# Optimization experiments

Hardware: AMD Instinct MI355X
Metric: run time of the kernel (lower is better)

Reference implementation:

```python
import jax, jax.numpy as jnp
import numpy as np
import math

IMAGE_SIZE = 300
STEPS = [16, 32, 64, 100, 150, 300]
MIN_SIZES = [60, 105, 150, 195, 240, 285]
MAX_SIZES = [105, 150, 195, 240, 285, 330]
ASPECT_RATIOS = [2, 3]
SCORE_THRESH = 0.02
NMS_THRESH = 0.45
POST_NMS_TOP_N = 100
VAR_XY, VAR_WH = 0.1, 0.2
BATCH, NUM_CLASSES = 16, 201


def _make_priors():
    # SSD-style anchor generation in (cx, cy, w, h), relative coords.
    priors = []
    for k, step in enumerate(STEPS):
        f = math.ceil(IMAGE_SIZE / step)
        s = MIN_SIZES[k] / IMAGE_SIZE
        sp = math.sqrt(MIN_SIZES[k] * MAX_SIZES[k]) / IMAGE_SIZE
        for i in range(f):
            for j in range(f):
                cx = (j + 0.5) * step / IMAGE_SIZE
                cy = (i + 0.5) * step / IMAGE_SIZE
                priors.append([cx, cy, s, s])
                priors.append([cx, cy, sp, sp])
                for ar in ASPECT_RATIOS:
                    r = math.sqrt(ar)
                    priors.append([cx, cy, s * r, s / r])
                    priors.append([cx, cy, s / r, s * r])
    return np.asarray(priors, dtype=np.float32)  # [3000, 4]


def setup_inputs() -> dict:
    key = jax.random.key(0)
    k1, k2 = jax.random.split(key)
    priors = jnp.asarray(_make_priors())  # [P, 4]
    P = priors.shape[0]
    pred_bbox_deltas = jax.random.normal(k1, (BATCH, P, 4), dtype=jnp.float32)
    objectness = jax.random.normal(k2, (BATCH, P, NUM_CLASSES), dtype=jnp.float32)
    return {"pred_bbox_deltas": pred_bbox_deltas, "objectness": objectness, "priors": priors}


def reference(pred_bbox_deltas, objectness, priors):
    # Eval path of MultiBoxHeads.filter_priors: softmax -> box decode ->
    # score filter -> class-aware (batched) NMS -> top-N, padded to fixed size.
    P = priors.shape[0]
    C = objectness.shape[-1]
    probs = jax.nn.softmax(objectness, axis=-1)  # [B, P, C]

    # BoxCoder.decode with variances (0.1, 0.2); priors are (cx, cy, w, h).
    pxy, pwh = priors[:, :2], priors[:, 2:]
    xy = pred_bbox_deltas[..., :2] * VAR_XY * pwh + pxy  # [B, P, 2]
    wh = jnp.exp(pred_bbox_deltas[..., 2:] * VAR_WH) * pwh
    decoded = jnp.concatenate([xy - 0.5 * wh, xy + 0.5 * wh], axis=-1)  # [B, P, 4] xyxy

    # Per-candidate class labels (background class 0 dropped), shared across images.
    labels = jnp.broadcast_to(jnp.arange(1, C), (P, C - 1)).reshape(-1)  # [P*(C-1)] int

    def nms_image(dec, prob):
        scores = prob[:, 1:].reshape(-1)  # [P*(C-1)]
        boxes = jnp.broadcast_to(dec[:, None, :], (P, C - 1, 4)).reshape(-1, 4)
        s = jnp.where(scores > SCORE_THRESH, scores, -1.0)
        # batched_nms trick: offset boxes by label so classes never overlap.
        off = jnp.max(boxes) + 1.0
        bo = boxes + labels.astype(boxes.dtype)[:, None] * off
        areas = (bo[:, 2] - bo[:, 0]) * (bo[:, 3] - bo[:, 1])

        def step(s, _):
            i = jnp.argmax(s)
            sc = s[i]
            b = bo[i]
            ix1 = jnp.maximum(bo[:, 0], b[0])
            iy1 = jnp.maximum(bo[:, 1], b[1])
            ix2 = jnp.minimum(bo[:, 2], b[2])
            iy2 = jnp.minimum(bo[:, 3], b[3])
            inter = jnp.clip(ix2 - ix1, 0.0) * jnp.clip(iy2 - iy1, 0.0)
            iou = inter / (areas + areas[i] - inter)
            s = jnp.where(iou > NMS_THRESH, -1.0, s).at[i].set(-1.0)
            return s, (i, sc)

        _, (idx, sc) = jax.lax.scan(step, s, None, length=POST_NMS_TOP_N)
        ok = sc > SCORE_THRESH  # slots that hold real detections
        b_out = jnp.where(ok[:, None], jnp.clip(boxes[idx], 0.0, 1.0), 0.0)  # parse() clamp
        s_out = jnp.where(ok, sc, 0.0)
        l_out = jnp.where(ok, labels[idx].astype(boxes.dtype), 0.0)
        # [K, 6] = (x1, y1, x2, y2, score, label); zero rows are padding.
        return jnp.concatenate([b_out, s_out[:, None], l_out[:, None]], axis=-1)

    return jax.vmap(nms_image)(decoded, probs)  # [B, POST_NMS_TOP_N, 6]
```

## Files before the change

kernel.cpp:

```cpp
#include <hip/hip_runtime.h>
#include <cfloat>
#include <cstdint>

#define BATCH 16
#define PRIORS 3000
#define NCLS 201
#define NLBL 200
#define TOPN 100
#define SCORE_THR 0.02f
#define NMS_THR 0.45f

#define FPPB 16
#define FBLK ((PRIORS + FPPB - 1) / FPPB)
#define SEGW 64
#define SEGS (FBLK * 4)
#define SLOTS (SEGS * SEGW)
#define HOTW 8
#define OVF_CAP 1024
#define T0 0.08f

#define NMS_T 1024
#define NBINS 1024
#define HCAP 512
#define SB_BASE 0x3CA3

__device__ __forceinline__ int key_stratum(uint64_t k) {
    int s = (int)(k >> 48) - SB_BASE;
    return s < 0 ? 0 : (s > NBINS - 1 ? NBINS - 1 : s);
}

__global__ __launch_bounds__(256) void score_filter_kernel(
    const float* __restrict__ obj,
    int*         __restrict__ cnt,
    int*         __restrict__ hcnt,
    uint64_t*    __restrict__ seg,
    uint64_t*    __restrict__ hot,
    uint64_t*    __restrict__ ovf,
    uint64_t*    __restrict__ hovf)
{
    const int b    = blockIdx.y;
    const int wave = threadIdx.x >> 6;
    const int lane = threadIdx.x & 63;
    const int segId = blockIdx.x * 4 + wave;
    uint64_t* myseg = seg + ((size_t)b * SEGS + segId) * SEGW;
    uint64_t* myhot = hot + ((size_t)b * SEGS + segId) * HOTW;
    const int pbase = blockIdx.x * FPPB + wave * 4;

    float v0[4], v1[4], v2[4], v3[4];
    bool pv[4];
#pragma unroll
    for (int pp = 0; pp < 4; ++pp) {
        int p = pbase + pp;
        pv[pp] = (p < PRIORS);
        const float* x = obj + ((size_t)b * PRIORS + (pv[pp] ? p : PRIORS - 1)) * NCLS;
        v0[pp] = x[lane];
        v1[pp] = x[lane + 64];
        v2[pp] = x[lane + 128];
        v3[pp] = (lane + 192 < NCLS) ? x[lane + 192] : -FLT_MAX;
    }
    float mx[4];
#pragma unroll
    for (int pp = 0; pp < 4; ++pp)
        mx[pp] = fmaxf(fmaxf(v0[pp], v1[pp]), fmaxf(v2[pp], v3[pp]));
    for (int d = 32; d > 0; d >>= 1) {
#pragma unroll
        for (int pp = 0; pp < 4; ++pp)
            mx[pp] = fmaxf(mx[pp], __shfl_xor(mx[pp], d, 64));
    }
    float e0[4], e1[4], e2[4], e3[4], se[4];
#pragma unroll
    for (int pp = 0; pp < 4; ++pp) {
        e0[pp] = expf(v0[pp] - mx[pp]);
        e1[pp] = expf(v1[pp] - mx[pp]);
        e2[pp] = expf(v2[pp] - mx[pp]);
        e3[pp] = (lane + 192 < NCLS) ? expf(v3[pp] - mx[pp]) : 0.0f;
        se[pp] = e0[pp] + e1[pp] + e2[pp] + e3[pp];
    }
    for (int d = 32; d > 0; d >>= 1) {
#pragma unroll
        for (int pp = 0; pp < 4; ++pp)
            se[pp] += __shfl_xor(se[pp], d, 64);
    }
    int cursor = 0, hcur = 0;
#pragma unroll
    for (int pp = 0; pp < 4; ++pp) {
        float inv = 1.0f / se[pp];
        int p = pbase + pp;
        float ev[4] = { e0[pp], e1[pp], e2[pp], e3[pp] };
#pragma unroll
        for (int k = 0; k < 4; ++k) {
            int c = lane + 64 * k;
            float prob = ev[k] * inv;
            bool pass = pv[pp] && (c >= 1) && (c < NCLS) && (prob > SCORE_THR);
            uint64_t mask = __ballot(pass);
            bool hotp = pass && (prob > T0);
            uint64_t hmask = __ballot(hotp);
            if (pass) {
                uint32_t oid = (uint32_t)(p * NLBL + (c - 1));
                uint64_t key = ((uint64_t)__float_as_uint(prob) << 32)
                             | (uint64_t)(0xFFFFFFFFu - oid);
                int idx = cursor + __popcll(mask & ((1ull << lane) - 1ull));
                if (idx < SEGW) {
                    myseg[idx] = key;
                } else {
                    int gi = atomicAdd(&cnt[b], 1);
                    if (gi < OVF_CAP) ovf[(size_t)b * OVF_CAP + gi] = key;
                }
                if (hotp) {
                    int hidx = hcur + __popcll(hmask & ((1ull << lane) - 1ull));
                    if (hidx < HOTW) {
                        myhot[hidx] = key;
                    } else {
                        int gi = atomicAdd(&hcnt[b], 1);
                        if (gi < OVF_CAP) hovf[(size_t)b * OVF_CAP + gi] = key;
                    }
                }
            }
            cursor += (int)__popcll(mask);
            hcur   += (int)__popcll(hmask);
        }
    }
    if (lane >= (cursor < SEGW ? cursor : SEGW)) myseg[lane] = 0ull;
    if (lane < HOTW && lane >= (hcur < HOTW ? hcur : HOTW)) myhot[lane] = 0ull;
}

__device__ __forceinline__ void sort512_desc(const uint64_t* skey,
                                             uint64_t K[8], int lane)
{
#pragma unroll
    for (int r = 0; r < 8; ++r) K[r] = skey[r * 64 + lane];
#pragma unroll
    for (int k2 = 2; k2 <= 512; k2 <<= 1) {
#pragma unroll
        for (int j2 = k2 >> 1; j2 >= 64; j2 >>= 1) {
            int j2r = j2 >> 6;
#pragma unroll
            for (int r = 0; r < 8; ++r) {
                if ((r & j2r) == 0) {
                    int rp = r | j2r;
                    bool up = ((((r << 6) + lane) & k2) == 0);
                    uint64_t a = K[r], bb = K[rp];
                    uint64_t mxk = a > bb ? a : bb;
                    uint64_t mnk = a > bb ? bb : a;
                    K[r]  = up ? mxk : mnk;
                    K[rp] = up ? mnk : mxk;
                }
            }
        }
#pragma unroll
        for (int j2 = ((k2 >> 1) < 32 ? (k2 >> 1) : 32); j2 >= 1; j2 >>= 1) {
#pragma unroll
            for (int r = 0; r < 8; ++r) {
                uint64_t o = __shfl_xor((unsigned long long)K[r], j2, 64);
                bool up = ((((r << 6) + lane) & k2) == 0);
                bool lower = ((lane & j2) == 0);
                K[r] = (up == lower) ? (K[r] > o ? K[r] : o)
                                     : (K[r] < o ? K[r] : o);
            }
        }
    }
}

__device__ __forceinline__ int scan_sorted_w0(
    const uint64_t K[8], int b, const float4* __restrict__ dbox, float ofb,
    float4* abox, float* aarea, int na, float* __restrict__ out, int lane)
{
#pragma unroll
    for (int r = 0; r < 8; ++r) {
        if (na >= TOPN) break;
        uint64_t myk = K[r];
        bool valid = (myk != 0ull);
        uint32_t oid = 0xFFFFFFFFu - (uint32_t)myk;
        int p = valid ? (int)(oid / NLBL) : 0;
        int c = valid ? ((int)(oid - (uint32_t)p * NLBL) + 1) : 1;
        float4 db = dbox[p];
        float lof = (float)c * ofb;
        float qx1 = db.x + lof, qy1 = db.y + lof;
        float qx2 = db.z + lof, qy2 = db.w + lof;
        float aq = (qx2 - qx1) * (qy2 - qy1);
        bool dead = false;
        for (int l = 0; l < na; ++l) {
            float4 a = abox[l];
            float ix1 = fmaxf(qx1, a.x), iy1 = fmaxf(qy1, a.y);
            float ix2 = fminf(qx2, a.z), iy2 = fminf(qy2, a.w);
            float inter = fmaxf(ix2 - ix1, 0.0f) * fmaxf(iy2 - iy1, 0.0f);
            float iou = inter / (aq + aarea[l] - inter);
            if (iou > NMS_THR) dead = true;
        }
        uint64_t alive = __ballot(valid && !dead);
        while (alive != 0ull && na < TOPN) {
            int j = __ffsll((unsigned long long)alive) - 1;
            float ax1 = __shfl(qx1, j, 64);
            float ay1 = __shfl(qy1, j, 64);
            float ax2 = __shfl(qx2, j, 64);
            float ay2 = __shfl(qy2, j, 64);
            float aa  = __shfl(aq,  j, 64);
            if (lane == j) {
                abox[na]  = make_float4(qx1, qy1, qx2, qy2);
                aarea[na] = aq;
                float* o = out + ((size_t)b * TOPN + na) * 6;
                o[0] = fminf(fmaxf(db.x, 0.0f), 1.0f);
                o[1] = fminf(fmaxf(db.y, 0.0f), 1.0f);
                o[2] = fminf(fmaxf(db.z, 0.0f), 1.0f);
                o[3] = fminf(fmaxf(db.w, 0.0f), 1.0f);
                o[4] = __uint_as_float((uint32_t)(myk >> 32));
                o[5] = (float)c;
            }
            na++;
            bool mine = ((alive >> lane) & 1ull) != 0ull;
            bool drop = (lane == j);
            if (mine && !drop) {
                float ix1 = fmaxf(qx1, ax1), iy1 = fmaxf(qy1, ay1);
                float ix2 = fminf(qx2, ax2), iy2 = fminf(qy2, ay2);
                float inter = fmaxf(ix2 - ix1, 0.0f) * fmaxf(iy2 - iy1, 0.0f);
                float iou = inter / (aq + aa - inter);
                if (iou > NMS_THR) drop = true;
            }
            alive = __ballot(mine && !drop);
        }
    }
    return na;
}

__device__ __forceinline__ int scan_step_w0(
    uint64_t key, int b, const float4* __restrict__ dbox, float ofb,
    float4* abox, float* aarea, int na, float* __restrict__ out, int lane)
{
    uint32_t oid = 0xFFFFFFFFu - (uint32_t)key;
    int p = (int)(oid / NLBL);
    int c = (int)(oid - (uint32_t)p * NLBL) + 1;
    float4 db = dbox[p];
    float lo = (float)c * ofb;
    float qx1 = db.x + lo, qy1 = db.y + lo;
    float qx2 = db.z + lo, qy2 = db.w + lo;
    float aq = (qx2 - qx1) * (qy2 - qy1);
    bool sup = false;
    for (int l = lane; l < na; l += 64) {
        float4 a = abox[l];
        float ix1 = fmaxf(qx1, a.x), iy1 = fmaxf(qy1, a.y);
        float ix2 = fminf(qx2, a.z), iy2 = fminf(qy2, a.w);
        float inter = fmaxf(ix2 - ix1, 0.0f) * fmaxf(iy2 - iy1, 0.0f);
        float iou = inter / (aq + aarea[l] - inter);
        if (iou > NMS_THR) sup = true;
    }
    if (__ballot(sup) == 0ull) {
        if (lane == 0) {
            abox[na]  = make_float4(qx1, qy1, qx2, qy2);
            aarea[na] = aq;
            float* o = out + ((size_t)b * TOPN + na) * 6;
            o[0] = fminf(fmaxf(db.x, 0.0f), 1.0f);
            o[1] = fminf(fmaxf(db.y, 0.0f), 1.0f);
            o[2] = fminf(fmaxf(db.z, 0.0f), 1.0f);
            o[3] = fminf(fmaxf(db.w, 0.0f), 1.0f);
            o[4] = __uint_as_float((uint32_t)(key >> 32));
            o[5] = (float)c;
        }
        __threadfence_block();
        return na + 1;
    }
    return na;
}

__global__ __launch_bounds__(NMS_T) void nms_kernel(
    const float*    __restrict__ deltas,
    const float*    __restrict__ priors,
    const int*      __restrict__ cnt,
    const int*      __restrict__ hcnt,
    const uint64_t* __restrict__ seg,
    const uint64_t* __restrict__ hot,
    const uint64_t* __restrict__ ovf,
    const uint64_t* __restrict__ hovf,
    float*          __restrict__ out)
{
    __shared__ float4   dbox[PRIORS];
    __shared__ int      sufx[NBINS];
    __shared__ uint64_t skey[HCAP];
    __shared__ float4   abox[112];
    __shared__ float    aarea[112];
    __shared__ uint64_t rk[NMS_T / 64];
    __shared__ float    wredF[NMS_T / 64];
    __shared__ int      wtotS[NMS_T / 64];
    __shared__ int      carryS[NMS_T / 64];
    __shared__ int cntC, loS, naS;
    __shared__ uint64_t fkS;

    const int b    = blockIdx.x;
    const int tid  = threadIdx.x;
    const int wave = tid >> 6;
    const int lane = tid & 63;
    const uint64_t* slots  = seg  + (size_t)b * SLOTS;
    const uint64_t* hslots = hot  + (size_t)b * SEGS * HOTW;
    int n_ovf  = cnt[b];  if (n_ovf  > OVF_CAP) n_ovf  = OVF_CAP;
    int n_hovf = hcnt[b]; if (n_hovf > OVF_CAP) n_hovf = OVF_CAP;
    const uint64_t* ovfp  = ovf  + (size_t)b * OVF_CAP;
    const uint64_t* hovfp = hovf + (size_t)b * OVF_CAP;

    if (tid == 0) { cntC = 0; naS = 0; }
    if (lane == 0) wredF[wave] = -FLT_MAX;
    __syncthreads();

    for (int j = tid; j < SEGS * HOTW; j += NMS_T) {
        uint64_t k = hslots[j];
        if (k) { int i = atomicAdd(&cntC, 1); if (i < HCAP) skey[i] = k; }
    }
    for (int j = tid; j < n_hovf; j += NMS_T) {
        uint64_t k = hovfp[j];
        if (k) { int i = atomicAdd(&cntC, 1); if (i < HCAP) skey[i] = k; }
    }
    __syncthreads();
    int hc = cntC;
    bool decoded = false;
    if (hc <= HCAP) {
        if (tid < HCAP && tid >= hc) skey[tid] = 0ull;
        __syncthreads();
        if (wave == 0) {
            uint64_t K[8];
            sort512_desc(skey, K, lane);
            __syncthreads();
            float ofb;
            {
                float v = (lane < NMS_T / 64) ? wredF[lane] : -FLT_MAX;
                for (int d = 32; d > 0; d >>= 1) v = fmaxf(v, __shfl_xor(v, d, 64));
                ofb = v + 1.0f;
            }
            int na = scan_sorted_w0(K, b, dbox, ofb, abox, aarea, 0, out, lane);
            if (lane == 0) naS = na;
        } else {
            int base0 = (wave - 1) * 200;
            float lmax = -FLT_MAX;
            for (int p = base0 + lane; p < base0 + 200; p += 64) {
                float4 d4 = ((const float4*)deltas)[(size_t)b * PRIORS + p];
                float4 pr = ((const float4*)priors)[p];
                float cx = d4.x * 0.1f * pr.z + pr.x;
                float cy = d4.y * 0.1f * pr.w + pr.y;
                float w  = expf(d4.z * 0.2f) * pr.z;
                float h  = expf(d4.w * 0.2f) * pr.w;
                float x1 = cx - 0.5f * w, y1 = cy - 0.5f * h;
                float x2 = cx + 0.5f * w, y2 = cy + 0.5f * h;
                dbox[p] = make_float4(x1, y1, x2, y2);
                lmax = fmaxf(lmax, fmaxf(fmaxf(x1, y1), fmaxf(x2, y2)));
            }
            for (int d = 32; d > 0; d >>= 1)
                lmax = fmaxf(lmax, __shfl_xor(lmax, d, 64));
            if (lane == 0) wredF[wave] = lmax;
            __syncthreads();
        }
        decoded = true;
        __syncthreads();
    }

    if (naS < TOPN) {
        if (!decoded) {
            float lmax = -FLT_MAX;
            for (int p = tid; p < PRIORS; p += NMS_T) {
                float4 d4 = ((const float4*)deltas)[(size_t)b * PRIORS + p];
                float4 pr = ((const float4*)priors)[p];
                float cx = d4.x * 0.1f * pr.z + pr.x;
                float cy = d4.y * 0.1f * pr.w + pr.y;
                float w  = expf(d4.z * 0.2f) * pr.z;
                float h  = expf(d4.w * 0.2f) * pr.w;
                float x1 = cx - 0.5f * w, y1 = cy - 0.5f * h;
                float x2 = cx + 0.5f * w, y2 = cy + 0.5f * h;
                dbox[p] = make_float4(x1, y1, x2, y2);
                lmax = fmaxf(lmax, fmaxf(fmaxf(x1, y1), fmaxf(x2, y2)));
            }
            for (int d = 32; d > 0; d >>= 1)
                lmax = fmaxf(lmax, __shfl_xor(lmax, d, 64));
            if (lane == 0) wredF[wave] = lmax;
        }
        sufx[tid] = 0;
        if (tid == 0) naS = 0;
        __syncthreads();
        for (int j = tid; j < SLOTS; j += NMS_T) {
            uint64_t k = slots[j];
            if (k) atomicAdd(&sufx[key_stratum(k)], 1);
        }
        for (int j = tid; j < n_ovf; j += NMS_T) {
            uint64_t k = ovfp[j];
            if (k) atomicAdd(&sufx[key_stratum(k)], 1);
        }
        __syncthreads();
        {
            int v = sufx[64 * wave + lane];
            int s = v;
            for (int d = 1; d < 64; d <<= 1) {
                int t = __shfl_down(s, d, 64);
                if (lane + d < 64) s += t;
            }
            if (lane == 0) wtotS[wave] = s;
            __syncthreads();
            if (wave == 0 && lane < NMS_T / 64) {
                int tv = wtotS[lane];
                int ts = tv;
                for (int d = 1; d < NMS_T / 64; d <<= 1) {
                    int t = __shfl_down(ts, d, 64);
                    if (lane + d < NMS_T / 64) ts += t;
                }
                carryS[lane] = ts - tv;
            }
            __syncthreads();
            sufx[64 * wave + lane] = s + carryS[wave];
        }
        int curHi = NBINS;
        for (;;) {
            __syncthreads();
            int naCur = naS;
            int A = (curHi < NBINS) ? sufx[curHi] : 0;
            int remaining = sufx[0] - A;
            if (naCur >= TOPN || remaining <= 0 || curHi <= 0) break;
            int target = A + HCAP;
            if (tid == 0) { loS = curHi; cntC = 0; }
            __syncthreads();
            if (tid < curHi) {
                if (sufx[tid] <= target && (tid == 0 || sufx[tid - 1] > target))
                    loS = tid;
            }
            __syncthreads();
            int lo = loS;

            if (lo < curHi) {
                for (int j = tid; j < SLOTS; j += NMS_T) {
                    uint64_t k = slots[j];
                    if (k) {
                        int s = key_stratum(k);
                        if (s >= lo && s < curHi) {
                            int i = atomicAdd(&cntC, 1);
                            if (i < HCAP) skey[i] = k;
                        }
                    }
                }
                for (int j = tid; j < n_ovf; j += NMS_T) {
                    uint64_t k = ovfp[j];
                    if (k) {
                        int s = key_stratum(k);
                        if (s >= lo && s < curHi) {
                            int i = atomicAdd(&cntC, 1);
                            if (i < HCAP) skey[i] = k;
                        }
                    }
                }
                __syncthreads();
                if (tid < HCAP && tid >= cntC) skey[tid] = 0ull;
                __syncthreads();
                if (wave == 0) {
                    uint64_t K[8];
                    sort512_desc(skey, K, lane);
                    float ofb;
                    {
                        float v = (lane < NMS_T / 64) ? wredF[lane] : -FLT_MAX;
                        for (int d = 32; d > 0; d >>= 1) v = fmaxf(v, __shfl_xor(v, d, 64));
                        ofb = v + 1.0f;
                    }
                    int na = scan_sorted_w0(K, b, dbox, ofb, abox, aarea, naS, out, lane);
                    if (lane == 0) naS = na;
                }
                curHi = lo;
            } else {
                float ofbT;
                {
                    float v = (lane < NMS_T / 64) ? wredF[lane] : -FLT_MAX;
                    for (int d = 32; d > 0; d >>= 1) v = fmaxf(v, __shfl_xor(v, d, 64));
                    ofbT = v + 1.0f;
                }
                int s = curHi - 1;
                uint64_t lastK = ~0ull;
                for (;;) {
                    __syncthreads();
                    if (naS >= TOPN) break;
                    uint64_t bk = 0ull;
                    for (int j = tid; j < SLOTS; j += NMS_T) {
                        uint64_t k = slots[j];
                        if (k && key_stratum(k) == s && k < lastK && k > bk) bk = k;
                    }
                    for (int j = tid; j < n_ovf; j += NMS_T) {
                        uint64_t k = ovfp[j];
                        if (k && key_stratum(k) == s && k < lastK && k > bk) bk = k;
                    }
                    for (int d = 32; d > 0; d >>= 1) {
                        uint64_t o = __shfl_xor((unsigned long long)bk, d, 64);
                        bk = (o > bk) ? o : bk;
                    }
                    if (lane == 0) rk[wave] = bk;
                    __syncthreads();
                    if (tid == 0) {
                        uint64_t fk = rk[0];
                        for (int w = 1; w < NMS_T / 64; ++w) fk = (rk[w] > fk) ? rk[w] : fk;
                        fkS = fk;
                    }
                    __syncthreads();
                    uint64_t fk = fkS;
                    if (fk == 0ull) break;
                    if (wave == 0) {
                        int nal = naS;
                        nal = scan_step_w0(fk, b, dbox, ofbT, abox, aarea, nal, out, lane);
                        if (lane == 0) naS = nal;
                    }
                    lastK = fk;
                }
                curHi = s;
            }
        }
    }
    __syncthreads();
    int naF = naS;
    for (int idx = tid; idx < (TOPN - naF) * 6; idx += NMS_T)
        out[(size_t)b * TOPN * 6 + (size_t)naF * 6 + idx] = 0.0f;
}

extern "C" void kernel_launch(void* const* d_in, const int* in_sizes, int n_in,
                              void* d_out, int out_size, void* d_ws, size_t ws_size,
                              hipStream_t stream)
{
    const float* deltas = (const float*)d_in[0];
    const float* obj    = (const float*)d_in[1];
    const float* priors = (const float*)d_in[2];
    float* out = (float*)d_out;

    char* ws = (char*)d_ws;
    int*      cnt  = (int*)ws;
    int*      hcnt = (int*)(ws + 64);
    uint64_t* hotA = (uint64_t*)(ws + 256);
    uint64_t* segA = hotA + (size_t)BATCH * SEGS * HOTW;
    uint64_t* ovfA = segA + (size_t)BATCH * SLOTS;
    uint64_t* hovA = ovfA + (size_t)BATCH * OVF_CAP;

    hipMemsetAsync(ws, 0, 128, stream);
    dim3 fg(FBLK, BATCH, 1);
    score_filter_kernel<<<fg, 256, 0, stream>>>(obj, cnt, hcnt, segA, hotA, ovfA, hovA);
    nms_kernel<<<BATCH, NMS_T, 0, stream>>>(deltas, priors, cnt, hcnt,
                                            segA, hotA, ovfA, hovA, out);
}
```

Baseline: 134.6 us.

## Vectorize score-filter loads and precompute per-chunk IoU suppression masks

The score filter now reads a wave's four contiguous priors as 201 float4 loads and works out each element's prior and class index from its flat position, instead of issuing strided scalar loads per prior. In the NMS scan, each 64-candidate chunk gets a full 64x64 IoU bitmask computed up front, so the serial survivor loop only does bit tests instead of shuffles and an IoU per accepted box. The shared key buffer is zeroed before collection, which removes one barrier. The matrix precompute always does 64 IoU rows even when few candidates survive, and the flat indexing adds select logic per element.

After: 140.3 us. 4.2% more time.

```diff
diff --git a/kernel.cpp b/kernel.cpp
--- a/kernel.cpp
+++ b/kernel.cpp
@@ -44,59 +44,94 @@
     const int segId = blockIdx.x * 4 + wave;
     uint64_t* myseg = seg + ((size_t)b * SEGS + segId) * SEGW;
     uint64_t* myhot = hot + ((size_t)b * SEGS + segId) * HOTW;
-    const int pbase = blockIdx.x * FPPB + wave * 4;
-
-    float v0[4], v1[4], v2[4], v3[4];
-    bool pv[4];
-#pragma unroll
-    for (int pp = 0; pp < 4; ++pp) {
-        int p = pbase + pp;
-        pv[pp] = (p < PRIORS);
-        const float* x = obj + ((size_t)b * PRIORS + (pv[pp] ? p : PRIORS - 1)) * NCLS;
-        v0[pp] = x[lane];
-        v1[pp] = x[lane + 64];
-        v2[pp] = x[lane + 128];
-        v3[pp] = (lane + 192 < NCLS) ? x[lane + 192] : -FLT_MAX;
-    }
-    float mx[4];
-#pragma unroll
-    for (int pp = 0; pp < 4; ++pp)
-        mx[pp] = fmaxf(fmaxf(v0[pp], v1[pp]), fmaxf(v2[pp], v3[pp]));
+    const int p0 = blockIdx.x * FPPB + wave * 4;
+
+    if (p0 >= PRIORS) {
+        myseg[lane] = 0ull;
+        if (lane < HOTW) myhot[lane] = 0ull;
+        return;
+    }
+
+    const float4* x4 = (const float4*)(obj + ((size_t)b * PRIORS + p0) * NCLS);
+    float4 q[4];
+#pragma unroll
+    for (int r = 0; r < 4; ++r) {
+        int f = r * 64 + lane;
+        q[r] = (f < 201) ? x4[f]
+                         : make_float4(-FLT_MAX, -FLT_MAX, -FLT_MAX, -FLT_MAX);
+    }
+
+    float mx[4] = { -FLT_MAX, -FLT_MAX, -FLT_MAX, -FLT_MAX };
+#pragma unroll
+    for (int r = 0; r < 4; ++r) {
+        const float* v = (const float*)&q[r];
+        int e0 = (r * 64 + lane) * 4;
+#pragma unroll
+        for (int i = 0; i < 4; ++i) {
+            int e = e0 + i;
+            int pe = (e >= 603) ? 3 : (e >= 402) ? 2 : (e >= 201) ? 1 : 0;
+#pragma unroll
+            for (int j = 0; j < 4; ++j)
+                if (pe == j) mx[j] = fmaxf(mx[j], v[i]);
+        }
+    }
     for (int d = 32; d > 0; d >>= 1) {
 #pragma unroll
-        for (int pp = 0; pp < 4; ++pp)
-            mx[pp] = fmaxf(mx[pp], __shfl_xor(mx[pp], d, 64));
-    }
-    float e0[4], e1[4], e2[4], e3[4], se[4];
-#pragma unroll
-    for (int pp = 0; pp < 4; ++pp) {
-        e0[pp] = expf(v0[pp] - mx[pp]);
-        e1[pp] = expf(v1[pp] - mx[pp]);
-        e2[pp] = expf(v2[pp] - mx[pp]);
-        e3[pp] = (lane + 192 < NCLS) ? expf(v3[pp] - mx[pp]) : 0.0f;
-        se[pp] = e0[pp] + e1[pp] + e2[pp] + e3[pp];
+        for (int j = 0; j < 4; ++j)
+            mx[j] = fmaxf(mx[j], __shfl_xor(mx[j], d, 64));
+    }
+#pragma unroll
+    for (int r = 0; r < 4; ++r) {
+        float* v = (float*)&q[r];
+        int e0 = (r * 64 + lane) * 4;
+#pragma unroll
+        for (int i = 0; i < 4; ++i) {
+            int e = e0 + i;
+            int pe = (e >= 603) ? 3 : (e >= 402) ? 2 : (e >= 201) ? 1 : 0;
+            float m = (pe == 3) ? mx[3] : (pe == 2) ? mx[2]
+                     : (pe == 1) ? mx[1] : mx[0];
+            v[i] = expf(v[i] - m);
+        }
+    }
+    float se[4] = { 0.0f, 0.0f, 0.0f, 0.0f };
+#pragma unroll
+    for (int r = 0; r < 4; ++r) {
+        const float* v = (const float*)&q[r];
+        int e0 = (r * 64 + lane) * 4;
+#pragma unroll
+        for (int i = 0; i < 4; ++i) {
+            int e = e0 + i;
+            int pe = (e >= 603) ? 3 : (e >= 402) ? 2 : (e >= 201) ? 1 : 0;
+#pragma unroll
+            for (int j = 0; j < 4; ++j)
+                if (pe == j) se[j] += v[i];
+        }
     }
     for (int d = 32; d > 0; d >>= 1) {
 #pragma unroll
-        for (int pp = 0; pp < 4; ++pp)
-            se[pp] += __shfl_xor(se[pp], d, 64);
-    }
+        for (int j = 0; j < 4; ++j)
+            se[j] += __shfl_xor(se[j], d, 64);
+    }
+    float inv[4] = { 1.0f / se[0], 1.0f / se[1], 1.0f / se[2], 1.0f / se[3] };
+
     int cursor = 0, hcur = 0;
 #pragma unroll
-    for (int pp = 0; pp < 4; ++pp) {
-        float inv = 1.0f / se[pp];
-        int p = pbase + pp;
-        float ev[4] = { e0[pp], e1[pp], e2[pp], e3[pp] };
-#pragma unroll
-        for (int k = 0; k < 4; ++k) {
-            int c = lane + 64 * k;
-            float prob = ev[k] * inv;
-            bool pass = pv[pp] && (c >= 1) && (c < NCLS) && (prob > SCORE_THR);
+    for (int r = 0; r < 4; ++r) {
+        const float* v = (const float*)&q[r];
+        int e0 = (r * 64 + lane) * 4;
+#pragma unroll
+        for (int i = 0; i < 4; ++i) {
+            int e = e0 + i;
+            int pe = (e >= 603) ? 3 : (e >= 402) ? 2 : (e >= 201) ? 1 : 0;
+            int ce = e - pe * 201;
+            float prob = v[i] * ((pe == 3) ? inv[3] : (pe == 2) ? inv[2]
+                               : (pe == 1) ? inv[1] : inv[0]);
+            bool pass = (e < 804) && (ce >= 1) && (prob > SCORE_THR);
             uint64_t mask = __ballot(pass);
             bool hotp = pass && (prob > T0);
             uint64_t hmask = __ballot(hotp);
             if (pass) {
-                uint32_t oid = (uint32_t)(p * NLBL + (c - 1));
+                uint32_t oid = (uint32_t)((p0 + pe) * NLBL + (ce - 1));
                 uint64_t key = ((uint64_t)__float_as_uint(prob) << 32)
                              | (uint64_t)(0xFFFFFFFFu - oid);
                 int idx = cursor + __popcll(mask & ((1ull << lane) - 1ull));
@@ -161,7 +196,7 @@
     }
 }
 
-__device__ __forceinline__ int scan_sorted_w0(
+__device__ __forceinline__ int scan_matrix_w0(
     const uint64_t K[8], int b, const float4* __restrict__ dbox, float ofb,
     float4* abox, float* aarea, int na, float* __restrict__ out, int lane)
 {
@@ -187,14 +222,25 @@
             float iou = inter / (aq + aarea[l] - inter);
             if (iou > NMS_THR) dead = true;
         }
-        uint64_t alive = __ballot(valid && !dead);
+        bool aliveB = valid && !dead;
+        uint64_t alive = __ballot(aliveB);
+        if (alive == 0ull) continue;
+        uint64_t M = 0ull;
+#pragma unroll 4
+        for (int jj = 0; jj < 64; ++jj) {
+            float ax1 = __shfl(qx1, jj, 64);
+            float ay1 = __shfl(qy1, jj, 64);
+            float ax2 = __shfl(qx2, jj, 64);
+            float ay2 = __shfl(qy2, jj, 64);
+            float aa  = __shfl(aq,  jj, 64);
+            float ix1 = fmaxf(qx1, ax1), iy1 = fmaxf(qy1, ay1);
+            float ix2 = fminf(qx2, ax2), iy2 = fminf(qy2, ay2);
+            float inter = fmaxf(ix2 - ix1, 0.0f) * fmaxf(iy2 - iy1, 0.0f);
+            float iou = inter / (aq + aa - inter);
+            if (iou > NMS_THR) M |= (1ull << jj);
+        }
         while (alive != 0ull && na < TOPN) {
             int j = __ffsll((unsigned long long)alive) - 1;
-            float ax1 = __shfl(qx1, j, 64);
-            float ay1 = __shfl(qy1, j, 64);
-            float ax2 = __shfl(qx2, j, 64);
-            float ay2 = __shfl(qy2, j, 64);
-            float aa  = __shfl(aq,  j, 64);
             if (lane == j) {
                 abox[na]  = make_float4(qx1, qy1, qx2, qy2);
                 aarea[na] = aq;
@@ -207,19 +253,18 @@
                 o[5] = (float)c;
             }
             na++;
-            bool mine = ((alive >> lane) & 1ull) != 0ull;
-            bool drop = (lane == j);
-            if (mine && !drop) {
-                float ix1 = fmaxf(qx1, ax1), iy1 = fmaxf(qy1, ay1);
-                float ix2 = fminf(qx2, ax2), iy2 = fminf(qy2, ay2);
-                float inter = fmaxf(ix2 - ix1, 0.0f) * fmaxf(iy2 - iy1, 0.0f);
-                float iou = inter / (aq + aa - inter);
-                if (iou > NMS_THR) drop = true;
-            }
-            alive = __ballot(mine && !drop);
+            aliveB = aliveB && !((M >> j) & 1ull);
+            alive = __ballot(aliveB);
         }
     }
     return na;
+}
+
+__device__ __forceinline__ int scan_sorted_w0(
+    const uint64_t K[8], int b, const float4* __restrict__ dbox, float ofb,
+    float4* abox, float* aarea, int na, float* __restrict__ out, int lane)
+{
+    return scan_matrix_w0(K, b, dbox, ofb, abox, aarea, na, out, lane);
 }
 
 __device__ __forceinline__ int scan_step_w0(
@@ -297,6 +342,7 @@
 
     if (tid == 0) { cntC = 0; naS = 0; }
     if (lane == 0) wredF[wave] = -FLT_MAX;
+    if (tid < HCAP) skey[tid] = 0ull;
     __syncthreads();
 
     for (int j = tid; j < SEGS * HOTW; j += NMS_T) {
@@ -311,8 +357,6 @@
     int hc = cntC;
     bool decoded = false;
     if (hc <= HCAP) {
-        if (tid < HCAP && tid >= hc) skey[tid] = 0ull;
-        __syncthreads();
         if (wave == 0) {
             uint64_t K[8];
             sort512_desc(skey, K, lane);
@@ -323,7 +367,7 @@
                 for (int d = 32; d > 0; d >>= 1) v = fmaxf(v, __shfl_xor(v, d, 64));
                 ofb = v + 1.0f;
             }
-            int na = scan_sorted_w0(K, b, dbox, ofb, abox, aarea, 0, out, lane);
+            int na = scan_matrix_w0(K, b, dbox, ofb, abox, aarea, 0, out, lane);
             if (lane == 0) naS = na;
         } else {
             int base0 = (wave - 1) * 200;
```

## Fuse score filter and NMS into one kernel with per-block done flags

Applied to the files above, without the earlier changes.

Merges the softmax/score-filter kernel and the NMS kernel into a single launch. Filter blocks grow to 1024 threads covering 64 priors each and publish per-block done flags with release stores. The trailing per-image NMS blocks decode boxes first, then spin on those flags, which overlaps box decode with filtering and removes a kernel boundary. The hot-candidate scan now precomputes a 64x64 IoU suppression bitmask per chunk instead of shuffling and recomputing IoU for each accepted box. The spin-wait assumes the filter blocks get scheduled before or alongside the NMS blocks, which the higher block indices make likely but not guaranteed.

New measurement: 415.8 us. 3.09x slower.

```diff
diff --git a/kernel.cpp b/kernel.cpp
--- a/kernel.cpp
+++ b/kernel.cpp
@@ -10,10 +10,10 @@
 #define SCORE_THR 0.02f
 #define NMS_THR 0.45f
 
-#define FPPB 16
+#define FPPB 64
 #define FBLK ((PRIORS + FPPB - 1) / FPPB)
 #define SEGW 64
-#define SEGS (FBLK * 4)
+#define SEGS (FBLK * 16)
 #define SLOTS (SEGS * SEGW)
 #define HOTW 8
 #define OVF_CAP 1024
@@ -23,105 +23,11 @@
 #define NBINS 1024
 #define HCAP 512
 #define SB_BASE 0x3CA3
+#define DONE_MAGIC 0x13579BDF
 
 __device__ __forceinline__ int key_stratum(uint64_t k) {
     int s = (int)(k >> 48) - SB_BASE;
     return s < 0 ? 0 : (s > NBINS - 1 ? NBINS - 1 : s);
-}
-
-__global__ __launch_bounds__(256) void score_filter_kernel(
-    const float* __restrict__ obj,
-    int*         __restrict__ cnt,
-    int*         __restrict__ hcnt,
-    uint64_t*    __restrict__ seg,
-    uint64_t*    __restrict__ hot,
-    uint64_t*    __restrict__ ovf,
-    uint64_t*    __restrict__ hovf)
-{
-    const int b    = blockIdx.y;
-    const int wave = threadIdx.x >> 6;
-    const int lane = threadIdx.x & 63;
-    const int segId = blockIdx.x * 4 + wave;
-    uint64_t* myseg = seg + ((size_t)b * SEGS + segId) * SEGW;
-    uint64_t* myhot = hot + ((size_t)b * SEGS + segId) * HOTW;
-    const int pbase = blockIdx.x * FPPB + wave * 4;
-
-    float v0[4], v1[4], v2[4], v3[4];
-    bool pv[4];
-#pragma unroll
-    for (int pp = 0; pp < 4; ++pp) {
-        int p = pbase + pp;
-        pv[pp] = (p < PRIORS);
-        const float* x = obj + ((size_t)b * PRIORS + (pv[pp] ? p : PRIORS - 1)) * NCLS;
-        v0[pp] = x[lane];
-        v1[pp] = x[lane + 64];
-        v2[pp] = x[lane + 128];
-        v3[pp] = (lane + 192 < NCLS) ? x[lane + 192] : -FLT_MAX;
-    }
-    float mx[4];
-#pragma unroll
-    for (int pp = 0; pp < 4; ++pp)
-        mx[pp] = fmaxf(fmaxf(v0[pp], v1[pp]), fmaxf(v2[pp], v3[pp]));
-    for (int d = 32; d > 0; d >>= 1) {
-#pragma unroll
-        for (int pp = 0; pp < 4; ++pp)
-            mx[pp] = fmaxf(mx[pp], __shfl_xor(mx[pp], d, 64));
-    }
-    float e0[4], e1[4], e2[4], e3[4], se[4];
-#pragma unroll
-    for (int pp = 0; pp < 4; ++pp) {
-        e0[pp] = expf(v0[pp] - mx[pp]);
-        e1[pp] = expf(v1[pp] - mx[pp]);
-        e2[pp] = expf(v2[pp] - mx[pp]);
-        e3[pp] = (lane + 192 < NCLS) ? expf(v3[pp] - mx[pp]) : 0.0f;
-        se[pp] = e0[pp] + e1[pp] + e2[pp] + e3[pp];
-    }
-    for (int d = 32; d > 0; d >>= 1) {
-#pragma unroll
-        for (int pp = 0; pp < 4; ++pp)
-            se[pp] += __shfl_xor(se[pp], d, 64);
-    }
-    int cursor = 0, hcur = 0;
-#pragma unroll
-    for (int pp = 0; pp < 4; ++pp) {
-        float inv = 1.0f / se[pp];
-        int p = pbase + pp;
-        float ev[4] = { e0[pp], e1[pp], e2[pp], e3[pp] };
-#pragma unroll
-        for (int k = 0; k < 4; ++k) {
-            int c = lane + 64 * k;
-            float prob = ev[k] * inv;
-            bool pass = pv[pp] && (c >= 1) && (c < NCLS) && (prob > SCORE_THR);
-            uint64_t mask = __ballot(pass);
-            bool hotp = pass && (prob > T0);
-            uint64_t hmask = __ballot(hotp);
-            if (pass) {
-                uint32_t oid = (uint32_t)(p * NLBL + (c - 1));
-                uint64_t key = ((uint64_t)__float_as_uint(prob) << 32)
-                             | (uint64_t)(0xFFFFFFFFu - oid);
-                int idx = cursor + __popcll(mask & ((1ull << lane) - 1ull));
-                if (idx < SEGW) {
-                    myseg[idx] = key;
-                } else {
-                    int gi = atomicAdd(&cnt[b], 1);
-                    if (gi < OVF_CAP) ovf[(size_t)b * OVF_CAP + gi] = key;
-                }
-                if (hotp) {
-                    int hidx = hcur + __popcll(hmask & ((1ull << lane) - 1ull));
-                    if (hidx < HOTW) {
-                        myhot[hidx] = key;
-                    } else {
-                        int gi = atomicAdd(&hcnt[b], 1);
-                        if (gi < OVF_CAP) hovf[(size_t)b * OVF_CAP + gi] = key;
-                    }
-                }
-            }
-            cursor += (int)__popcll(mask);
-            hcur   += (int)__popcll(hmask);
-        }
-    }
-    if (lane >= (cursor < SEGW ? cursor : SEGW)) myseg[lane] = 0ull;
-    if (lane < HOTW && lane >= (hcur < HOTW ? hcur : HOTW)) myhot[lane] = 0ull;
 }
 
 __device__ __forceinline__ void sort512_desc(const uint64_t* skey,
@@ -161,7 +67,7 @@
     }
 }
 
-__device__ __forceinline__ int scan_sorted_w0(
+__device__ __forceinline__ int scan_matrix_w0(
     const uint64_t K[8], int b, const float4* __restrict__ dbox, float ofb,
     float4* abox, float* aarea, int na, float* __restrict__ out, int lane)
 {
@@ -187,14 +93,25 @@
             float iou = inter / (aq + aarea[l] - inter);
             if (iou > NMS_THR) dead = true;
         }
-        uint64_t alive = __ballot(valid && !dead);
+        bool aliveB = valid && !dead;
+        uint64_t alive = __ballot(aliveB);
+        if (alive == 0ull) continue;
+        uint64_t M = 0ull;
+#pragma unroll 4
+        for (int jj = 0; jj < 64; ++jj) {
+            float ax1 = __shfl(qx1, jj, 64);
+            float ay1 = __shfl(qy1, jj, 64);
+            float ax2 = __shfl(qx2, jj, 64);
+            float ay2 = __shfl(qy2, jj, 64);
+            float aa  = __shfl(aq,  jj, 64);
+            float ix1 = fmaxf(qx1, ax1), iy1 = fmaxf(qy1, ay1);
+            float ix2 = fminf(qx2, ax2), iy2 = fminf(qy2, ay2);
+            float inter = fmaxf(ix2 - ix1, 0.0f) * fmaxf(iy2 - iy1, 0.0f);
+            float iou = inter / (aq + aa - inter);
+            if (iou > NMS_THR) M |= (1ull << jj);
+        }
         while (alive != 0ull && na < TOPN) {
             int j = __ffsll((unsigned long long)alive) - 1;
-            float ax1 = __shfl(qx1, j, 64);
-            float ay1 = __shfl(qy1, j, 64);
-            float ax2 = __shfl(qx2, j, 64);
-            float ay2 = __shfl(qy2, j, 64);
-            float aa  = __shfl(aq,  j, 64);
             if (lane == j) {
                 abox[na]  = make_float4(qx1, qy1, qx2, qy2);
                 aarea[na] = aq;
@@ -207,16 +124,8 @@
                 o[5] = (float)c;
             }
             na++;
-            bool mine = ((alive >> lane) & 1ull) != 0ull;
-            bool drop = (lane == j);
-            if (mine && !drop) {
-                float ix1 = fmaxf(qx1, ax1), iy1 = fmaxf(qy1, ay1);
-                float ix2 = fminf(qx2, ax2), iy2 = fminf(qy2, ay2);
-                float inter = fmaxf(ix2 - ix1, 0.0f) * fmaxf(iy2 - iy1, 0.0f);
-                float iou = inter / (aq + aa - inter);
-                if (iou > NMS_THR) drop = true;
-            }
-            alive = __ballot(mine && !drop);
+            aliveB = aliveB && !((M >> j) & 1ull);
+            alive = __ballot(aliveB);
         }
     }
     return na;
@@ -261,16 +170,18 @@
     return na;
 }
 
-__global__ __launch_bounds__(NMS_T) void nms_kernel(
-    const float*    __restrict__ deltas,
-    const float*    __restrict__ priors,
-    const int*      __restrict__ cnt,
-    const int*      __restrict__ hcnt,
-    const uint64_t* __restrict__ seg,
-    const uint64_t* __restrict__ hot,
-    const uint64_t* __restrict__ ovf,
-    const uint64_t* __restrict__ hovf,
-    float*          __restrict__ out)
+__global__ __launch_bounds__(NMS_T) void fused_kernel(
+    const float* __restrict__ obj,
+    const float* __restrict__ deltas,
+    const float* __restrict__ priors,
+    int*         __restrict__ cnt,
+    int*         __restrict__ hcnt,
+    int*         __restrict__ doneF,
+    uint64_t*    __restrict__ seg,
+    uint64_t*    __restrict__ hot,
+    uint64_t*    __restrict__ ovf,
+    uint64_t*    __restrict__ hovf,
+    float*       __restrict__ out)
 {
     __shared__ float4   dbox[PRIORS];
     __shared__ int      sufx[NBINS];
@@ -284,20 +195,149 @@
     __shared__ int cntC, loS, naS;
     __shared__ uint64_t fkS;
 
-    const int b    = blockIdx.x;
     const int tid  = threadIdx.x;
     const int wave = tid >> 6;
     const int lane = tid & 63;
-    const uint64_t* slots  = seg  + (size_t)b * SLOTS;
-    const uint64_t* hslots = hot  + (size_t)b * SEGS * HOTW;
+
+    if (blockIdx.x < FBLK * BATCH) {
+        const int fb = blockIdx.x;
+        const int b = fb / FBLK, blk = fb % FBLK;
+        const int segId = blk * 16 + wave;
+        uint64_t* myseg = seg + ((size_t)b * SEGS + segId) * SEGW;
+        uint64_t* myhot = hot + ((size_t)b * SEGS + segId) * HOTW;
+        const int pbase = blk * FPPB + wave * 4;
+
+        float v0[4], v1[4], v2[4], v3[4];
+        bool pv[4];
+#pragma unroll
+        for (int pp = 0; pp < 4; ++pp) {
+            int p = pbase + pp;
+            pv[pp] = (p < PRIORS);
+            const float* x = obj + ((size_t)b * PRIORS + (pv[pp] ? p : PRIORS - 1)) * NCLS;
+            v0[pp] = x[lane];
+            v1[pp] = x[lane + 64];
+            v2[pp] = x[lane + 128];
+            v3[pp] = (lane + 192 < NCLS) ? x[lane + 192] : -FLT_MAX;
+        }
+        float mx[4];
+#pragma unroll
+        for (int pp = 0; pp < 4; ++pp)
+            mx[pp] = fmaxf(fmaxf(v0[pp], v1[pp]), fmaxf(v2[pp], v3[pp]));
+        for (int d = 32; d > 0; d >>= 1) {
+#pragma unroll
+            for (int pp = 0; pp < 4; ++pp)
+                mx[pp] = fmaxf(mx[pp], __shfl_xor(mx[pp], d, 64));
+        }
+        float e0[4], e1[4], e2[4], e3[4], se[4];
+#pragma unroll
+        for (int pp = 0; pp < 4; ++pp) {
+            e0[pp] = expf(v0[pp] - mx[pp]);
+            e1[pp] = expf(v1[pp] - mx[pp]);
+            e2[pp] = expf(v2[pp] - mx[pp]);
+            e3[pp] = (lane + 192 < NCLS) ? expf(v3[pp] - mx[pp]) : 0.0f;
+            se[pp] = e0[pp] + e1[pp] + e2[pp] + e3[pp];
+        }
+        for (int d = 32; d > 0; d >>= 1) {
+#pragma unroll
+            for (int pp = 0; pp < 4; ++pp)
+                se[pp] += __shfl_xor(se[pp], d, 64);
+        }
+        int cursor = 0, hcur = 0;
+#pragma unroll
+        for (int pp = 0; pp < 4; ++pp) {
+            float inv = 1.0f / se[pp];
+            int p = pbase + pp;
+            float ev[4] = { e0[pp], e1[pp], e2[pp], e3[pp] };
+#pragma unroll
+            for (int k = 0; k < 4; ++k) {
+                int c = lane + 64 * k;
+                float prob = ev[k] * inv;
+                bool pass = pv[pp] && (c >= 1) && (c < NCLS) && (prob > SCORE_THR);
+                uint64_t mask = __ballot(pass);
+                bool hotp = pass && (prob > T0);
+                uint64_t hmask = __ballot(hotp);
+                if (pass) {
+                    uint32_t oid = (uint32_t)(p * NLBL + (c - 1));
+                    uint64_t key = ((uint64_t)__float_as_uint(prob) << 32)
+                                 | (uint64_t)(0xFFFFFFFFu - oid);
+                    int idx = cursor + __popcll(mask & ((1ull << lane) - 1ull));
+                    if (idx < SEGW) {
+                        myseg[idx] = key;
+                    } else {
+                        int gi = atomicAdd(&cnt[b], 1);
+                        if (gi < OVF_CAP) ovf[(size_t)b * OVF_CAP + gi] = key;
+                    }
+                    if (hotp) {
+                        int hidx = hcur + __popcll(hmask & ((1ull << lane) - 1ull));
+                        if (hidx < HOTW) {
+                            myhot[hidx] = key;
+                        } else {
+                            int gi = atomicAdd(&hcnt[b], 1);
+                            if (gi < OVF_CAP) hovf[(size_t)b * OVF_CAP + gi] = key;
+                        }
+                    }
+                }
+                cursor += (int)__popcll(mask);
+                hcur   += (int)__popcll(hmask);
+            }
+        }
+        if (lane >= (cursor < SEGW ? cursor : SEGW)) myseg[lane] = 0ull;
+        if (lane < HOTW && lane >= (hcur < HOTW ? hcur : HOTW)) myhot[lane] = 0ull;
+
+        __threadfence();
+        __syncthreads();
+        if (tid == 0)
+            __hip_atomic_store(&doneF[b * FBLK + blk], DONE_MAGIC,
+                               __ATOMIC_RELEASE, __HIP_MEMORY_SCOPE_AGENT);
+        return;
+    }
+
+    const int b = blockIdx.x - FBLK * BATCH;
+    const uint64_t* slots  = seg + (size_t)b * SLOTS;
+    const uint64_t* hslots = hot + (size_t)b * SEGS * HOTW;
+    const uint64_t* ovfp   = ovf  + (size_t)b * OVF_CAP;
+    const uint64_t* hovfp  = hovf + (size_t)b * OVF_CAP;
+
+    if (tid == 0) { cntC = 0; naS = 0; }
+    if (tid < HCAP) skey[tid] = 0ull;
+
+    float lmax = -FLT_MAX;
+    for (int p = tid; p < PRIORS; p += NMS_T) {
+        float4 d4 = ((const float4*)deltas)[(size_t)b * PRIORS + p];
+        float4 pr = ((const float4*)priors)[p];
+        float cx = d4.x * 0.1f * pr.z + pr.x;
+        float cy = d4.y * 0.1f * pr.w + pr.y;
+        float w  = expf(d4.z * 0.2f) * pr.z;
+        float h  = expf(d4.w * 0.2f) * pr.w;
+        float x1 = cx - 0.5f * w, y1 = cy - 0.5f * h;
+        float x2 = cx + 0.5f * w, y2 = cy + 0.5f * h;
+        dbox[p] = make_float4(x1, y1, x2, y2);
+        lmax = fmaxf(lmax, fmaxf(fmaxf(x1, y1), fmaxf(x2, y2)));
+    }
+    for (int d = 32; d > 0; d >>= 1)
+        lmax = fmaxf(lmax, __shfl_xor(lmax, d, 64));
+    if (lane == 0) wredF[wave] = lmax;
+    __syncthreads();
+    float ofb;
+    {
+        float v = (lane < NMS_T / 64) ? wredF[lane] : -FLT_MAX;
+        for (int d = 32; d > 0; d >>= 1) v = fmaxf(v, __shfl_xor(v, d, 64));
+        ofb = v + 1.0f;
+    }
+
+    {
+        const int* df = doneF + b * FBLK;
+        for (;;) {
+            int v = (lane < FBLK)
+                  ? __hip_atomic_load(&df[lane], __ATOMIC_ACQUIRE,
+                                      __HIP_MEMORY_SCOPE_AGENT)
+                  : DONE_MAGIC;
+            if (__ballot(v == DONE_MAGIC) == ~0ull) break;
+            __builtin_amdgcn_s_sleep(2);
+        }
+    }
     int n_ovf  = cnt[b];  if (n_ovf  > OVF_CAP) n_ovf  = OVF_CAP;
     int n_hovf = hcnt[b]; if (n_hovf > OVF_CAP) n_hovf = OVF_CAP;
-    const uint64_t* ovfp  = ovf  + (size_t)b * OVF_CAP;
-    const uint64_t* hovfp = hovf + (size_t)b * OVF_CAP;
-
-    if (tid == 0) { cntC = 0; naS = 0; }
-    if (lane == 0) wredF[wave] = -FLT_MAX;
-    __syncthreads();
 
     for (int j = tid; j < SEGS * HOTW; j += NMS_T) {
         uint64_t k = hslots[j];
@@ -309,65 +349,17 @@
     }
     __syncthreads();
     int hc = cntC;
-    bool decoded = false;
     if (hc <= HCAP) {
-        if (tid < HCAP && tid >= hc) skey[tid] = 0ull;
-        __syncthreads();
         if (wave == 0) {
             uint64_t K[8];
             sort512_desc(skey, K, lane);
-            __syncthreads();
-            float ofb;
-            {
-                float v = (lane < NMS_T / 64) ? wredF[lane] : -FLT_MAX;
-                for (int d = 32; d > 0; d >>= 1) v = fmaxf(v, __shfl_xor(v, d, 64));
-                ofb = v + 1.0f;
-            }
-            int na = scan_sorted_w0(K, b, dbox, ofb, abox, aarea, 0, out, lane);
+            int na = scan_matrix_w0(K, b, dbox, ofb, abox, aarea, 0, out, lane);
             if (lane == 0) naS = na;
-        } else {
-            int base0 = (wave - 1) * 200;
-            float lmax = -FLT_MAX;
-            for (int p = base0 + lane; p < base0 + 200; p += 64) {
-                float4 d4 = ((const float4*)deltas)[(size_t)b * PRIORS + p];
-                float4 pr = ((const float4*)priors)[p];
-                float cx = d4.x * 0.1f * pr.z + pr.x;
-                float cy = d4.y * 0.1f * pr.w + pr.y;
-                float w  = expf(d4.z * 0.2f) * pr.z;
-                float h  = expf(d4.w * 0.2f) * pr.w;
-                float x1 = cx - 0.5f * w, y1 = cy - 0.5f * h;
-                float x2 = cx + 0.5f * w, y2 = cy + 0.5f * h;
-                dbox[p] = make_float4(x1, y1, x2, y2);
-                lmax = fmaxf(lmax, fmaxf(fmaxf(x1, y1), fmaxf(x2, y2)));
-            }
-            for (int d = 32; d > 0; d >>= 1)
-                lmax = fmaxf(lmax, __shfl_xor(lmax, d, 64));
-            if (lane == 0) wredF[wave] = lmax;
-            __syncthreads();
-        }
-        decoded = true;
-        __syncthreads();
-    }
+        }
+    }
+    __syncthreads();
 
     if (naS < TOPN) {
-        if (!decoded) {
-            float lmax = -FLT_MAX;
-            for (int p = tid; p < PRIORS; p += NMS_T) {
-                float4 d4 = ((const float4*)deltas)[(size_t)b * PRIORS + p];
-                float4 pr = ((const float4*)priors)[p];
-                float cx = d4.x * 0.1f * pr.z + pr.x;
-                float cy = d4.y * 0.1f * pr.w + pr.y;
-                float w  = expf(d4.z * 0.2f) * pr.z;
-                float h  = expf(d4.w * 0.2f) * pr.w;
-                float x1 = cx - 0.5f * w, y1 = cy - 0.5f * h;
-                float x2 = cx + 0.5f * w, y2 = cy + 0.5f * h;
-                dbox[p] = make_float4(x1, y1, x2, y2);
-                lmax = fmaxf(lmax, fmaxf(fmaxf(x1, y1), fmaxf(x2, y2)));
-            }
-            for (int d = 32; d > 0; d >>= 1)
-                lmax = fmaxf(lmax, __shfl_xor(lmax, d, 64));
-            if (lane == 0) wredF[wave] = lmax;
-        }
         sufx[tid] = 0;
         if (tid == 0) naS = 0;
         __syncthreads();
@@ -445,23 +437,11 @@
                 if (wave == 0) {
                     uint64_t K[8];
                     sort512_desc(skey, K, lane);
-                    float ofb;
-                    {
-                        float v = (lane < NMS_T / 64) ? wredF[lane] : -FLT_MAX;
-                        for (int d = 32; d > 0; d >>= 1) v = fmaxf(v, __shfl_xor(v, d, 64));
-                        ofb = v + 1.0f;
-                    }
-                    int na = scan_sorted_w0(K, b, dbox, ofb, abox, aarea, naS, out, lane);
+                    int na = scan_matrix_w0(K, b, dbox, ofb, abox, aarea, naS, out, lane);
                     if (lane == 0) naS = na;
                 }
                 curHi = lo;
             } else {
-                float ofbT;
-                {
-                    float v = (lane < NMS_T / 64) ? wredF[lane] : -FLT_MAX;
-                    for (int d = 32; d > 0; d >>= 1) v = fmaxf(v, __shfl_xor(v, d, 64));
-                    ofbT = v + 1.0f;
-                }
                 int s = curHi - 1;
                 uint64_t lastK = ~0ull;
                 for (;;) {
@@ -492,7 +472,7 @@
                     if (fk == 0ull) break;
                     if (wave == 0) {
                         int nal = naS;
-                        nal = scan_step_w0(fk, b, dbox, ofbT, abox, aarea, nal, out, lane);
+                        nal = scan_step_w0(fk, b, dbox, ofb, abox, aarea, nal, out, lane);
                         if (lane == 0) naS = nal;
                     }
                     lastK = fk;
@@ -500,8 +480,8 @@
                 curHi = s;
             }
         }
-    }
-    __syncthreads();
+        __syncthreads();
+    }
     int naF = naS;
     for (int idx = tid; idx < (TOPN - naF) * 6; idx += NMS_T)
         out[(size_t)b * TOPN * 6 + (size_t)naF * 6 + idx] = 0.0f;
@@ -517,16 +497,17 @@
     float* out = (float*)d_out;
 
     char* ws = (char*)d_ws;
-    int*      cnt  = (int*)ws;
-    int*      hcnt = (int*)(ws + 64);
-    uint64_t* hotA = (uint64_t*)(ws + 256);
+    int*      cnt   = (int*)ws;
+    int*      hcnt  = (int*)(ws + 64);
+    int*      doneF = (int*)(ws + 128);
+    size_t    zBytes = 128 + (size_t)BATCH * FBLK * 4;
+    size_t    off    = (zBytes + 255) & ~(size_t)255;
+    uint64_t* hotA = (uint64_t*)(ws + off);
     uint64_t* segA = hotA + (size_t)BATCH * SEGS * HOTW;
     uint64_t* ovfA = segA + (size_t)BATCH * SLOTS;
     uint64_t* hovA = ovfA + (size_t)BATCH * OVF_CAP;
 
-    hipMemsetAsync(ws, 0, 128, stream);
-    dim3 fg(FBLK, BATCH, 1);
-    score_filter_kernel<<<fg, 256, 0, stream>>>(obj, cnt, hcnt, segA, hotA, ovfA, hovA);
-    nms_kernel<<<BATCH, NMS_T, 0, stream>>>(deltas, priors, cnt, hcnt,
-                                            segA, hotA, ovfA, hovA, out);
+    hipMemsetAsync(ws, 0, zBytes, stream);
+    fused_kernel<<<FBLK * BATCH + BATCH, NMS_T, 0, stream>>>(
+        obj, deltas, priors, cnt, hcnt, doneF, segA, hotA, ovfA, hovA, out);
 }
```
